# Optimization experiments

Measured on AMD Instinct MI355X. Metric: run time of the kernel, lower is better.

## Reference

```python
import jax, jax.numpy as jnp
import numpy as np

N_NODES = 100000
N_EDGES = 1600000
IN_CH = 128
OUT_CH = 128
N_REL = 64
N_BASES = 8


def setup_inputs() -> dict:
    key = jax.random.key(0)
    k = jax.random.split(key, 7)
    x = jax.random.normal(k[0], (N_NODES, IN_CH), dtype=jnp.float32)
    src = jax.random.randint(k[1], (N_EDGES,), 0, N_NODES, dtype=jnp.int32)
    rel = jax.random.randint(k[2], (N_EDGES,), 0, N_REL, dtype=jnp.int32)
    dst = jax.random.randint(k[3], (N_EDGES,), 0, N_NODES, dtype=jnp.int32)
    edge_triples = jnp.stack([src, rel, dst], axis=1)  # [E, 3] (src, rel, dst)
    # xavier-uniform-ish scales
    basis = jax.random.normal(k[4], (N_BASES, IN_CH, OUT_CH), dtype=jnp.float32) * (2.0 / (IN_CH + OUT_CH)) ** 0.5
    att = jax.random.normal(k[5], (N_REL, N_BASES), dtype=jnp.float32) * (2.0 / (N_REL + N_BASES)) ** 0.5
    root_w = jax.random.normal(k[6], (IN_CH, OUT_CH), dtype=jnp.float32) * (1.0 / IN_CH) ** 0.5
    root_b = jnp.zeros((OUT_CH,), dtype=jnp.float32)
    return {"x": x, "edge_triples": edge_triples, "num_nodes": N_NODES,
            "basis": basis, "att": att, "root_w": root_w, "root_b": root_b}


def reference(x, edge_triples, num_nodes, basis, att, root_w, root_b):
    src = edge_triples[:, 0]
    rel = edge_triples[:, 1]
    dst = edge_triples[:, 2]
    att_e = att[rel]  # [E, B]
    n_bases = basis.shape[0]
    e = src.shape[0]
    out_ch = basis.shape[2]
    # messages[e] = x[src[e]] @ (sum_b att[rel[e], b] * basis[b])
    # computed as sum_b att_e[:, b] * (x @ basis[b])[src] to avoid the huge
    # per-edge [E, in, out] weight gather the torch code materializes.
    msgs = jnp.zeros((e, out_ch), dtype=x.dtype)
    for b in range(n_bases):  # small fixed loop over bases
        yb = x @ basis[b]  # [N, out]
        msgs = msgs + att_e[:, b:b + 1] * yb[src]
    # degree normalization (mean aggregation over incoming edges)
    deg = jax.ops.segment_sum(jnp.ones((e,), dtype=x.dtype), dst, num_segments=num_nodes)
    deg_inv = jnp.where(deg > 0, 1.0 / deg, 0.0)
    msgs = msgs * deg_inv[dst][:, None]
    agg = jax.ops.segment_sum(msgs, dst, num_segments=num_nodes)  # [N, out]
    return agg + x @ root_w + root_b
```

## Files before the change

### kernel.cpp

```cpp
#include <hip/hip_runtime.h>

#define NCH 128
#define NREL 64
#define NBP 1024
#define ESB 4096
#define CAPF 3072
#define KTOT 1152
#define KST 36
#define ZROW 2304

typedef __attribute__((ext_vector_type(8))) short bf16x8;
typedef __attribute__((ext_vector_type(4))) float f32x4;

__device__ __forceinline__ unsigned short f2bf(float f) {
    unsigned u = __float_as_uint(f);
    return (unsigned short)((u + 0x7fffu + ((u >> 16) & 1u)) >> 16);
}
__device__ __forceinline__ unsigned pack2bf(float a, float b) {
    return (unsigned)f2bf(a) | ((unsigned)f2bf(b) << 16);
}

__global__ __launch_bounds__(256) void k_prep(const float* __restrict__ x,
                                              unsigned short* __restrict__ x_bf,
                                              long total8) {
    long i = (long)blockIdx.x * 256 + threadIdx.x;
    if (i >= total8) return;
    const float4* xp = (const float4*)x;
    float4 v0 = xp[i * 2], v1 = xp[i * 2 + 1];
    bf16x8 p;
    p[0] = (short)f2bf(v0.x); p[1] = (short)f2bf(v0.y);
    p[2] = (short)f2bf(v0.z); p[3] = (short)f2bf(v0.w);
    p[4] = (short)f2bf(v1.x); p[5] = (short)f2bf(v1.y);
    p[6] = (short)f2bf(v1.z); p[7] = (short)f2bf(v1.w);
    ((bf16x8*)x_bf)[i] = p;
}

__global__ __launch_bounds__(256) void k_buildB(const float* __restrict__ basis,
                                                const float* __restrict__ att,
                                                const float* __restrict__ rw,
                                                float* __restrict__ attc,
                                                unsigned short* __restrict__ basisP) {
    int idx = blockIdx.x * 256 + threadIdx.x;
    if (idx < 512) attc[idx] = att[idx];
    if (idx >= 128 * KTOT) return;
    int j = idx & 7, lg = (idx >> 3) & 3, oc = (idx >> 5) & 127, kk = idx >> 12;
    int k = kk * 32 + lg * 8 + j;
    float v = (k < 1024) ? basis[(size_t)(k >> 7) * NCH * NCH + (size_t)(k & 127) * NCH + oc]
                         : rw[(size_t)(k - 1024) * NCH + oc];
    basisP[idx] = f2bf(v);
}

__global__ __launch_bounds__(256) void k_count(const int* __restrict__ trip, int E, int NB,
                                               int* __restrict__ cntB) {
    __shared__ int hb[NBP];
    int t = threadIdx.x;
    for (int i = t; i < NB; i += 256) hb[i] = 0;
    __syncthreads();
    int base = blockIdx.x * ESB;
#pragma unroll
    for (int i = 0; i < ESB / 256; ++i) {
        int e = base + i * 256 + t;
        if (e < E) atomicAdd(&hb[trip[3 * e + 2] >> 7], 1);
    }
    __syncthreads();
    for (int i = t; i < NB; i += 256) cntB[(size_t)blockIdx.x * NB + i] = hb[i];
}

__global__ __launch_bounds__(1024) void k_scanB(int* __restrict__ cntB, int GB, int NB,
                                                int* __restrict__ bhist) {
    __shared__ int sc[1024];
    int t = threadIdx.x, b = blockIdx.x;
    int v = (t < GB) ? cntB[(size_t)t * NB + b] : 0;
    sc[t] = v;
    __syncthreads();
    for (int off = 1; off < 1024; off <<= 1) {
        int a = (t >= off) ? sc[t - off] : 0;
        __syncthreads();
        sc[t] += a;
        __syncthreads();
    }
    if (t < GB) cntB[(size_t)t * NB + b] = sc[t] - v;
    if (t == GB - 1) bhist[b] = sc[t];
}

__global__ __launch_bounds__(1024) void k_offsets(const int* __restrict__ bhist, int NB,
                                                  int* __restrict__ bucketoff) {
    __shared__ int sc[1024];
    int t = threadIdx.x;
    int d = (t < NB) ? bhist[t] : 0;
    sc[t] = d;
    __syncthreads();
    for (int off = 1; off < 1024; off <<= 1) {
        int a = (t >= off) ? sc[t - off] : 0;
        __syncthreads();
        sc[t] += a;
        __syncthreads();
    }
    if (t < NB) bucketoff[t] = sc[t] - d;
    if (t == NB - 1) bucketoff[NB] = sc[t];
}

__global__ __launch_bounds__(256) void k_scatter(const int* __restrict__ trip, int E, int NB,
                                                 const int* __restrict__ cntB,
                                                 const int* __restrict__ bucketoff,
                                                 unsigned* __restrict__ packed) {
    __shared__ int cb[NBP], lbase[NBP], delta[NBP];
    __shared__ int ssc[256];
    __shared__ unsigned lpk[ESB];
    __shared__ unsigned short lb[ESB];
    int t = threadIdx.x, blk = blockIdx.x;
    for (int i = t; i < NB; i += 256) cb[i] = 0;
    __syncthreads();
    int base = blk * ESB;
    int total = min(ESB, E - base);

    unsigned pk[ESB / 256];
    int rk[ESB / 256];
    unsigned short bk[ESB / 256];
#pragma unroll
    for (int i = 0; i < ESB / 256; ++i) {
        int e = base + i * 256 + t;
        pk[i] = 0; rk[i] = 0; bk[i] = 0;
        if (e < E) {
            int src = trip[3 * e], rel = trip[3 * e + 1], dst = trip[3 * e + 2];
            int bkt = dst >> 7;
            bk[i] = (unsigned short)bkt;
            pk[i] = ((unsigned)(dst & 127) << 23) | ((unsigned)rel << 17) | (unsigned)src;
            rk[i] = atomicAdd(&cb[bkt], 1);
        }
    }
    __syncthreads();
    int ch = (NB + 255) >> 8;
    int mysum = 0;
    for (int i = 0; i < ch; ++i) {
        int idx = t * ch + i;
        if (idx < NB) mysum += cb[idx];
    }
    ssc[t] = mysum;
    __syncthreads();
    for (int off = 1; off < 256; off <<= 1) {
        int a = (t >= off) ? ssc[t - off] : 0;
        __syncthreads();
        ssc[t] += a;
        __syncthreads();
    }
    int run = ssc[t] - mysum;
    for (int i = 0; i < ch; ++i) {
        int idx = t * ch + i;
        if (idx < NB) { lbase[idx] = run; run += cb[idx]; }
    }
    __syncthreads();
    for (int i = t; i < NB; i += 256)
        delta[i] = bucketoff[i] + cntB[(size_t)blk * NB + i] - lbase[i];
    __syncthreads();
#pragma unroll
    for (int i = 0; i < ESB / 256; ++i) {
        int e = base + i * 256 + t;
        if (e < E) {
            int j = lbase[bk[i]] + rk[i];
            lpk[j] = pk[i];
            lb[j] = bk[i];
        }
    }
    __syncthreads();
    for (int j = t; j < total; j += 256)
        packed[delta[lb[j]] + j] = lpk[j];
}

__global__ __launch_bounds__(512, 4) void k_fused(const unsigned* __restrict__ x32,
                                                  const unsigned* __restrict__ packed,
                                                  const int* __restrict__ bucketoff,
                                                  const float* __restrict__ attc,
                                                  const unsigned short* __restrict__ basisP,
                                                  const float* __restrict__ rb,
                                                  float* __restrict__ out, int N) {
    __shared__ bf16x8 ztV[16 * (ZROW / 16)];
    __shared__ unsigned sortedE[CAPF];
    __shared__ float attl[512];
    __shared__ int h[128], hs[128];
    char* zt = (char*)ztV;

    int t = threadIdx.x, b = blockIdx.x;
    int w = t >> 6, lane = t & 63, lr = lane & 15, lg = lane >> 4;

    if (t < 512) attl[t] = attc[t];
    if (t < 128) h[t] = 0;
    __syncthreads();

    int s0 = bucketoff[b], s1 = bucketoff[b + 1];
    int cnt = min(s1 - s0, CAPF);

    unsigned pk[CAPF / 512];
    int rk[CAPF / 512];
#pragma unroll
    for (int i = 0; i < CAPF / 512; ++i) {
        int j = i * 512 + t;
        pk[i] = 0; rk[i] = 0;
        if (j < cnt) {
            unsigned p = packed[s0 + j];
            pk[i] = p;
            rk[i] = atomicAdd(&h[p >> 23], 1);
        }
    }
    __syncthreads();
    if (t < 128) hs[t] = h[t];
    __syncthreads();
    for (int off = 1; off < 128; off <<= 1) {
        int a = (t < 128 && t >= off) ? hs[t - off] : 0;
        __syncthreads();
        if (t < 128) hs[t] += a;
        __syncthreads();
    }
#pragma unroll
    for (int i = 0; i < CAPF / 512; ++i) {
        int j = i * 512 + t;
        if (j < cnt) {
            int d = pk[i] >> 23;
            sortedE[hs[d] - h[d] + rk[i]] = pk[i];
        }
    }
    __syncthreads();

    float z[16];
#pragma unroll
    for (int i = 0; i < 16; ++i) z[i] = 0.f;

    for (int r = 0; r < 8; ++r) {
        int d0 = r * 16 + w * 2;
        int eBeg = hs[d0] - h[d0];
        int eEnd = hs[d0 + 1];
        int cur = d0;
        int bnd = hs[d0];

        auto FLUSH = [&](int d) {
            float inv = (h[d] > 0) ? 1.f / (float)h[d] : 0.f;
            int zr = d & 15;
            char* zrow = zt + zr * ZROW;
            int sw = zr & 7;
#pragma unroll
            for (int bb = 0; bb < 8; ++bb) {
                unsigned pq = pack2bf(z[2 * bb] * inv, z[2 * bb + 1] * inv);
                int unit = (bb * 16 + (lane >> 2)) ^ sw;
                *(unsigned*)(zrow + (unit << 4) + ((lane & 3) << 2)) = pq;
                z[2 * bb] = 0.f; z[2 * bb + 1] = 0.f;
            }
            int n = b * 128 + d;
            unsigned xv = (n < N) ? x32[(size_t)n * 64 + lane] : 0u;
            int unit = (128 + (lane >> 2)) ^ sw;
            *(unsigned*)(zrow + (unit << 4) + ((lane & 3) << 2)) = xv;
        };

        if (eBeg < eEnd) {
            int last = eEnd - 1;
            unsigned pkA[8], xvA[8], pkB[8], xvB[8];

            auto LOAD8 = [&](unsigned* pkX, unsigned* xvX, int base2) {
#pragma unroll
                for (int i = 0; i < 8; ++i) {
                    int e = base2 + i;
                    int ec = (e < last) ? e : last;
                    unsigned p = sortedE[ec];
                    pkX[i] = p;
                    xvX[i] = x32[(size_t)(p & 0x1FFFFu) * 64 + lane];
                }
            };
            auto CONSUME8 = [&](const unsigned* pkX, const unsigned* xvX, int base2) {
#pragma unroll
                for (int i = 0; i < 8; ++i) {
                    int e = base2 + i;
                    if (e < eEnd) {
                        while (e >= bnd) { FLUSH(cur); ++cur; bnd = hs[cur]; }
                        unsigned p = pkX[i];
                        unsigned xv = xvX[i];
                        int rel = (p >> 17) & 63;
                        f32x4 a0 = *(const f32x4*)&attl[rel * 8];
                        f32x4 a1 = *(const f32x4*)&attl[rel * 8 + 4];
                        float lo = __uint_as_float(xv << 16);
                        float hi = __uint_as_float(xv & 0xffff0000u);
                        z[0] += a0[0] * lo;  z[1] += a0[0] * hi;
                        z[2] += a0[1] * lo;  z[3] += a0[1] * hi;
                        z[4] += a0[2] * lo;  z[5] += a0[2] * hi;
                        z[6] += a0[3] * lo;  z[7] += a0[3] * hi;
                        z[8] += a1[0] * lo;  z[9] += a1[0] * hi;
                        z[10] += a1[1] * lo; z[11] += a1[1] * hi;
                        z[12] += a1[2] * lo; z[13] += a1[2] * hi;
                        z[14] += a1[3] * lo; z[15] += a1[3] * hi;
                    }
                }
            };

            LOAD8(pkA, xvA, eBeg);
            LOAD8(pkB, xvB, eBeg + 8);
            for (int e0 = eBeg; e0 < eEnd; e0 += 16) {
                CONSUME8(pkA, xvA, e0);
                LOAD8(pkA, xvA, e0 + 16);
                CONSUME8(pkB, xvB, e0 + 8);
                LOAD8(pkB, xvB, e0 + 24);
            }
        }
        while (cur < d0 + 2) { FLUSH(cur); ++cur; }
        __syncthreads();

        f32x4 acc = {0.f, 0.f, 0.f, 0.f};
        int ocr = w * 16 + lr;
        int sw = lr & 7;
#pragma unroll 6
        for (int kk = 0; kk < KST; ++kk) {
            bf16x8 a = *(const bf16x8*)(zt + lr * ZROW + ((((kk << 2) + lg) ^ sw) << 4));
            bf16x8 b0 = *(const bf16x8*)(basisP + ((((size_t)kk * 128 + ocr) * 4 + lg) << 3));
            acc = __builtin_amdgcn_mfma_f32_16x16x32_bf16(b0, a, acc, 0, 0, 0);
        }

        int n = b * 128 + r * 16 + lr;
        if (n < N) {
            int oc0 = w * 16 + lg * 4;
            f32x4 bias = *(const f32x4*)(rb + oc0);
            *(f32x4*)(out + (size_t)n * NCH + oc0) = acc + bias;
        }
        __syncthreads();
    }
}

extern "C" void kernel_launch(void* const* d_in, const int* in_sizes, int n_in,
                              void* d_out, int out_size, void* d_ws, size_t ws_size,
                              hipStream_t stream) {
    const float* x = (const float*)d_in[0];
    const int* trip = (const int*)d_in[1];
    const float* basis = (const float*)d_in[3];
    const float* att = (const float*)d_in[4];
    const float* rw = (const float*)d_in[5];
    const float* rb = (const float*)d_in[6];
    float* out = (float*)d_out;

    int N = in_sizes[0] / NCH;
    int E = in_sizes[1] / 3;
    int NB = (N + 127) >> 7;
    int GB = (E + ESB - 1) / ESB;

    char* ws = (char*)d_ws;
    size_t off = 0;
    auto alloc = [&](size_t bts) { size_t o = off; off = (off + bts + 255) & ~(size_t)255; return o; };
    size_t oXbf    = alloc((size_t)N * NCH * 2);
    size_t oBasisP = alloc((size_t)128 * KTOT * 2);
    size_t oAttc   = alloc(512 * 4);
    size_t oCntB   = alloc((size_t)GB * NB * 4);
    size_t oBhist  = alloc((NBP + 1) * 4);
    size_t oBktoff = alloc((NBP + 1) * 4);
    size_t oPacked = alloc((size_t)E * 4);
    (void)off; (void)ws_size;

    unsigned short* x_bf = (unsigned short*)(ws + oXbf);
    unsigned short* basisP = (unsigned short*)(ws + oBasisP);
    float* attc = (float*)(ws + oAttc);
    int* cntB = (int*)(ws + oCntB);
    int* bhist = (int*)(ws + oBhist);
    int* bucketoff = (int*)(ws + oBktoff);
    unsigned* packed = (unsigned*)(ws + oPacked);

    long total8 = (long)N * NCH / 8;
    k_prep<<<(int)((total8 + 255) / 256), 256, 0, stream>>>(x, x_bf, total8);
    k_buildB<<<(128 * KTOT + 255) / 256, 256, 0, stream>>>(basis, att, rw, attc, basisP);
    k_count<<<GB, 256, 0, stream>>>(trip, E, NB, cntB);
    k_scanB<<<NB, 1024, 0, stream>>>(cntB, GB, NB, bhist);
    k_offsets<<<1, 1024, 0, stream>>>(bhist, NB, bucketoff);
    k_scatter<<<GB, 256, 0, stream>>>(trip, E, NB, cntB, bucketoff, packed);
    k_fused<<<NB, 512, 0, stream>>>((const unsigned*)x_bf, packed, bucketoff, attc, basisP,
                                    rb, out, N);
}
```

Measured before the change: 310.9 us.

## Split per-bucket dst sort into separate kernel and dynamically assign rows to waves

The in-block counting sort of edges by destination moves out of the fused kernel into a new k_sortbkt kernel, which writes sorted edges and per-destination offsets to global memory. The fused kernel drops the sorted-edge LDS buffer and raises its occupancy hint to 8 blocks per CU. Inside each 16-row tile, waves now take destination rows one at a time through an LDS atomic counter instead of a fixed two rows each, to balance uneven degrees. In exchange it adds a kernel launch, an extra global round trip of the edge array, and an atomic plus shuffle per row.

```diff
diff --git a/kernel.cpp b/kernel.cpp
--- a/kernel.cpp
+++ b/kernel.cpp
@@ -167,73 +167,80 @@
         packed[delta[lb[j]] + j] = lpk[j];
 }
 
-__global__ __launch_bounds__(512, 4) void k_fused(const unsigned* __restrict__ x32,
-                                                  const unsigned* __restrict__ packed,
-                                                  const int* __restrict__ bucketoff,
+__global__ __launch_bounds__(256) void k_sortbkt(const unsigned* __restrict__ packed,
+                                                 const int* __restrict__ bucketoff,
+                                                 unsigned* __restrict__ sortedG,
+                                                 int* __restrict__ dstoffG) {
+    __shared__ int h[128], hs[128];
+    int t = threadIdx.x, b = blockIdx.x;
+    if (t < 128) h[t] = 0;
+    __syncthreads();
+    int s0 = bucketoff[b], s1 = bucketoff[b + 1];
+    int cnt = min(s1 - s0, CAPF);
+
+    unsigned pk[CAPF / 256];
+    int rk[CAPF / 256];
+#pragma unroll
+    for (int i = 0; i < CAPF / 256; ++i) {
+        int j = i * 256 + t;
+        pk[i] = 0; rk[i] = 0;
+        if (j < cnt) {
+            unsigned p = packed[s0 + j];
+            pk[i] = p;
+            rk[i] = atomicAdd(&h[p >> 23], 1);
+        }
+    }
+    __syncthreads();
+    if (t < 128) hs[t] = h[t];
+    __syncthreads();
+    for (int off = 1; off < 128; off <<= 1) {
+        int a = (t < 128 && t >= off) ? hs[t - off] : 0;
+        __syncthreads();
+        if (t < 128) hs[t] += a;
+        __syncthreads();
+    }
+    if (t < 128) dstoffG[b * 129 + t] = s0 + hs[t] - h[t];
+    if (t == 0) dstoffG[b * 129 + 128] = s0 + cnt;
+#pragma unroll
+    for (int i = 0; i < CAPF / 256; ++i) {
+        int j = i * 256 + t;
+        if (j < cnt) {
+            int d = pk[i] >> 23;
+            sortedG[s0 + hs[d] - h[d] + rk[i]] = pk[i];
+        }
+    }
+}
+
+__global__ __launch_bounds__(512, 8) void k_fused(const unsigned* __restrict__ x32,
+                                                  const unsigned* __restrict__ sortedG,
+                                                  const int* __restrict__ dstoffG,
                                                   const float* __restrict__ attc,
                                                   const unsigned short* __restrict__ basisP,
                                                   const float* __restrict__ rb,
                                                   float* __restrict__ out, int N) {
     __shared__ bf16x8 ztV[16 * (ZROW / 16)];
-    __shared__ unsigned sortedE[CAPF];
     __shared__ float attl[512];
-    __shared__ int h[128], hs[128];
+    __shared__ int nextD;
     char* zt = (char*)ztV;
 
     int t = threadIdx.x, b = blockIdx.x;
     int w = t >> 6, lane = t & 63, lr = lane & 15, lg = lane >> 4;
 
     if (t < 512) attl[t] = attc[t];
-    if (t < 128) h[t] = 0;
-    __syncthreads();
-
-    int s0 = bucketoff[b], s1 = bucketoff[b + 1];
-    int cnt = min(s1 - s0, CAPF);
-
-    unsigned pk[CAPF / 512];
-    int rk[CAPF / 512];
-#pragma unroll
-    for (int i = 0; i < CAPF / 512; ++i) {
-        int j = i * 512 + t;
-        pk[i] = 0; rk[i] = 0;
-        if (j < cnt) {
-            unsigned p = packed[s0 + j];
-            pk[i] = p;
-            rk[i] = atomicAdd(&h[p >> 23], 1);
-        }
-    }
-    __syncthreads();
-    if (t < 128) hs[t] = h[t];
-    __syncthreads();
-    for (int off = 1; off < 128; off <<= 1) {
-        int a = (t < 128 && t >= off) ? hs[t - off] : 0;
-        __syncthreads();
-        if (t < 128) hs[t] += a;
-        __syncthreads();
-    }
-#pragma unroll
-    for (int i = 0; i < CAPF / 512; ++i) {
-        int j = i * 512 + t;
-        if (j < cnt) {
-            int d = pk[i] >> 23;
-            sortedE[hs[d] - h[d] + rk[i]] = pk[i];
-        }
-    }
-    __syncthreads();
+    if (t == 0) nextD = 0;
+    __syncthreads();
+
+    const int* doffs = dstoffG + b * 129;
 
     float z[16];
 #pragma unroll
     for (int i = 0; i < 16; ++i) z[i] = 0.f;
 
     for (int r = 0; r < 8; ++r) {
-        int d0 = r * 16 + w * 2;
-        int eBeg = hs[d0] - h[d0];
-        int eEnd = hs[d0 + 1];
-        int cur = d0;
-        int bnd = hs[d0];
-
-        auto FLUSH = [&](int d) {
-            float inv = (h[d] > 0) ? 1.f / (float)h[d] : 0.f;
+        int rEnd = r * 16 + 16;
+
+        auto FLUSH = [&](int d, int cnt_d) {
+            float inv = (cnt_d > 0) ? 1.f / (float)cnt_d : 0.f;
             int zr = d & 15;
             char* zrow = zt + zr * ZROW;
             int sw = zr & 7;
@@ -250,55 +257,64 @@
             *(unsigned*)(zrow + (unit << 4) + ((lane & 3) << 2)) = xv;
         };
 
-        if (eBeg < eEnd) {
-            int last = eEnd - 1;
-            unsigned pkA[8], xvA[8], pkB[8], xvB[8];
-
-            auto LOAD8 = [&](unsigned* pkX, unsigned* xvX, int base2) {
-#pragma unroll
-                for (int i = 0; i < 8; ++i) {
-                    int e = base2 + i;
-                    int ec = (e < last) ? e : last;
-                    unsigned p = sortedE[ec];
-                    pkX[i] = p;
-                    xvX[i] = x32[(size_t)(p & 0x1FFFFu) * 64 + lane];
+        for (;;) {
+            int my = 0x7FFFFFFF;
+            if (lane == 0) my = atomicAdd(&nextD, 1);
+            my = __shfl(my, 0, 64);
+            if (my >= rEnd) break;
+            int d = my;
+            int eBeg = doffs[d], eEnd = doffs[d + 1];
+            int cnt_d = eEnd - eBeg;
+
+            if (cnt_d > 0) {
+                int last = eEnd - 1;
+                unsigned pkA[8], xvA[8], pkB[8], xvB[8];
+
+                auto LOAD8 = [&](unsigned* pkX, unsigned* xvX, int base2) {
+#pragma unroll
+                    for (int i = 0; i < 8; ++i) {
+                        int e = base2 + i;
+                        int ec = (e < last) ? e : last;
+                        unsigned p = sortedG[ec];
+                        pkX[i] = p;
+                        xvX[i] = x32[(size_t)(p & 0x1FFFFu) * 64 + lane];
+                    }
+                };
+                auto CONSUME8 = [&](const unsigned* pkX, const unsigned* xvX, int base2) {
+#pragma unroll
+                    for (int i = 0; i < 8; ++i) {
+                        int e = base2 + i;
+                        if (e < eEnd) {
+                            unsigned p = pkX[i];
+                            unsigned xv = xvX[i];
+                            int rel = (p >> 17) & 63;
+                            f32x4 a0 = *(const f32x4*)&attl[rel * 8];
+                            f32x4 a1 = *(const f32x4*)&attl[rel * 8 + 4];
+                            float lo = __uint_as_float(xv << 16);
+                            float hi = __uint_as_float(xv & 0xffff0000u);
+                            z[0] += a0[0] * lo;  z[1] += a0[0] * hi;
+                            z[2] += a0[1] * lo;  z[3] += a0[1] * hi;
+                            z[4] += a0[2] * lo;  z[5] += a0[2] * hi;
+                            z[6] += a0[3] * lo;  z[7] += a0[3] * hi;
+                            z[8] += a1[0] * lo;  z[9] += a1[0] * hi;
+                            z[10] += a1[1] * lo; z[11] += a1[1] * hi;
+                            z[12] += a1[2] * lo; z[13] += a1[2] * hi;
+                            z[14] += a1[3] * lo; z[15] += a1[3] * hi;
+                        }
+                    }
+                };
+
+                LOAD8(pkA, xvA, eBeg);
+                LOAD8(pkB, xvB, eBeg + 8);
+                for (int e0 = eBeg; e0 < eEnd; e0 += 16) {
+                    CONSUME8(pkA, xvA, e0);
+                    if (e0 + 16 < eEnd) LOAD8(pkA, xvA, e0 + 16);
+                    CONSUME8(pkB, xvB, e0 + 8);
+                    if (e0 + 24 < eEnd) LOAD8(pkB, xvB, e0 + 24);
                 }
-            };
-            auto CONSUME8 = [&](const unsigned* pkX, const unsigned* xvX, int base2) {
-#pragma unroll
-                for (int i = 0; i < 8; ++i) {
-                    int e = base2 + i;
-                    if (e < eEnd) {
-                        while (e >= bnd) { FLUSH(cur); ++cur; bnd = hs[cur]; }
-                        unsigned p = pkX[i];
-                        unsigned xv = xvX[i];
-                        int rel = (p >> 17) & 63;
-                        f32x4 a0 = *(const f32x4*)&attl[rel * 8];
-                        f32x4 a1 = *(const f32x4*)&attl[rel * 8 + 4];
-                        float lo = __uint_as_float(xv << 16);
-                        float hi = __uint_as_float(xv & 0xffff0000u);
-                        z[0] += a0[0] * lo;  z[1] += a0[0] * hi;
-                        z[2] += a0[1] * lo;  z[3] += a0[1] * hi;
-                        z[4] += a0[2] * lo;  z[5] += a0[2] * hi;
-                        z[6] += a0[3] * lo;  z[7] += a0[3] * hi;
-                        z[8] += a1[0] * lo;  z[9] += a1[0] * hi;
-                        z[10] += a1[1] * lo; z[11] += a1[1] * hi;
-                        z[12] += a1[2] * lo; z[13] += a1[2] * hi;
-                        z[14] += a1[3] * lo; z[15] += a1[3] * hi;
-                    }
-                }
-            };
-
-            LOAD8(pkA, xvA, eBeg);
-            LOAD8(pkB, xvB, eBeg + 8);
-            for (int e0 = eBeg; e0 < eEnd; e0 += 16) {
-                CONSUME8(pkA, xvA, e0);
-                LOAD8(pkA, xvA, e0 + 16);
-                CONSUME8(pkB, xvB, e0 + 8);
-                LOAD8(pkB, xvB, e0 + 24);
             }
-        }
-        while (cur < d0 + 2) { FLUSH(cur); ++cur; }
+            FLUSH(d, cnt_d);
+        }
         __syncthreads();
 
         f32x4 acc = {0.f, 0.f, 0.f, 0.f};
@@ -317,6 +333,7 @@
             f32x4 bias = *(const f32x4*)(rb + oc0);
             *(f32x4*)(out + (size_t)n * NCH + oc0) = acc + bias;
         }
+        if (t == 0) nextD = rEnd;
         __syncthreads();
     }
 }
@@ -347,6 +364,8 @@
     size_t oBhist  = alloc((NBP + 1) * 4);
     size_t oBktoff = alloc((NBP + 1) * 4);
     size_t oPacked = alloc((size_t)E * 4);
+    size_t oSorted = alloc((size_t)E * 4);
+    size_t oDoff   = alloc((size_t)NB * 129 * 4);
     (void)off; (void)ws_size;
 
     unsigned short* x_bf = (unsigned short*)(ws + oXbf);
@@ -356,6 +375,8 @@
     int* bhist = (int*)(ws + oBhist);
     int* bucketoff = (int*)(ws + oBktoff);
     unsigned* packed = (unsigned*)(ws + oPacked);
+    unsigned* sortedG = (unsigned*)(ws + oSorted);
+    int* dstoffG = (int*)(ws + oDoff);
 
     long total8 = (long)N * NCH / 8;
     k_prep<<<(int)((total8 + 255) / 256), 256, 0, stream>>>(x, x_bf, total8);
@@ -364,6 +385,7 @@
     k_scanB<<<NB, 1024, 0, stream>>>(cntB, GB, NB, bhist);
     k_offsets<<<1, 1024, 0, stream>>>(bhist, NB, bucketoff);
     k_scatter<<<GB, 256, 0, stream>>>(trip, E, NB, cntB, bucketoff, packed);
-    k_fused<<<NB, 512, 0, stream>>>((const unsigned*)x_bf, packed, bucketoff, attc, basisP,
+    k_sortbkt<<<NB, 256, 0, stream>>>(packed, bucketoff, sortedG, dstoffG);
+    k_fused<<<NB, 512, 0, stream>>>((const unsigned*)x_bf, sortedG, dstoffG, attc, basisP,
                                     rb, out, N);
 }
```

New measurement: 355.4 us. 1.14x slower.
